# Optimization experiments

Measured on AMD Instinct MI355X. Metric: run time of the kernel, lower is better.

The kernel has to match this reference:

```python
import jax, jax.numpy as jnp
import numpy as np

H = 20          # n_hidden
D_IN = 64       # max_len_input (encoder GRU input size)
VOCAB = 128     # decoder_dict_size
B = 8192
S = 128
MAX_DEC = 6


def _gru_cell(x, h, W_ih, W_hh, b_ih, b_hh):
    # PyTorch GRU cell: gates ordered [r, z, n]
    gi = x @ W_ih.T + b_ih
    gh = h @ W_hh.T + b_hh
    ir, iz, inn = jnp.split(gi, 3, axis=-1)
    hr, hz, hn = jnp.split(gh, 3, axis=-1)
    r = jax.nn.sigmoid(ir + hr)
    z = jax.nn.sigmoid(iz + hz)
    n = jnp.tanh(inn + r * hn)
    return (1.0 - z) * n + z * h


def setup_inputs() -> dict:
    key = jax.random.key(0)
    ks = jax.random.split(key, 32)
    s = 0.1
    p = {}
    p["x"] = jax.random.normal(ks[0], (B, S, D_IN), dtype=jnp.float32)
    # encoder GRU (2 layers)
    p["enc_Wih0"] = jax.random.normal(ks[1], (3 * H, D_IN)) * s
    p["enc_Whh0"] = jax.random.normal(ks[2], (3 * H, H)) * s
    p["enc_bih0"] = jax.random.normal(ks[3], (3 * H,)) * s
    p["enc_bhh0"] = jax.random.normal(ks[4], (3 * H,)) * s
    p["enc_Wih1"] = jax.random.normal(ks[5], (3 * H, H)) * s
    p["enc_Whh1"] = jax.random.normal(ks[6], (3 * H, H)) * s
    p["enc_bih1"] = jax.random.normal(ks[7], (3 * H,)) * s
    p["enc_bhh1"] = jax.random.normal(ks[8], (3 * H,)) * s
    # decoder GRU (2 layers, input size H)
    p["dec_Wih0"] = jax.random.normal(ks[9], (3 * H, H)) * s
    p["dec_Whh0"] = jax.random.normal(ks[10], (3 * H, H)) * s
    p["dec_bih0"] = jax.random.normal(ks[11], (3 * H,)) * s
    p["dec_bhh0"] = jax.random.normal(ks[12], (3 * H,)) * s
    p["dec_Wih1"] = jax.random.normal(ks[13], (3 * H, H)) * s
    p["dec_Whh1"] = jax.random.normal(ks[14], (3 * H, H)) * s
    p["dec_bih1"] = jax.random.normal(ks[15], (3 * H,)) * s
    p["dec_bhh1"] = jax.random.normal(ks[16], (3 * H,)) * s
    # embedding / attention / output heads
    p["emb"] = jax.random.normal(ks[17], (VOCAB, H)) * s
    p["q_W"] = jax.random.normal(ks[18], (H, H)) * s
    p["q_b"] = jax.random.normal(ks[19], (H,)) * s
    p["comb_W"] = jax.random.normal(ks[20], (H, 2 * H)) * s
    p["comb_b"] = jax.random.normal(ks[21], (H,)) * s
    p["out_W"] = jax.random.normal(ks[22], (VOCAB, H)) * s
    p["out_b"] = jax.random.normal(ks[23], (VOCAB,)) * s
    return p


def reference(x, enc_Wih0, enc_Whh0, enc_bih0, enc_bhh0,
              enc_Wih1, enc_Whh1, enc_bih1, enc_bhh1,
              dec_Wih0, dec_Whh0, dec_bih0, dec_bhh0,
              dec_Wih1, dec_Whh1, dec_bih1, dec_bhh1,
              emb, q_W, q_b, comb_W, comb_b, out_W, out_b):
    b = x.shape[0]
    h0 = jnp.zeros((b, H), x.dtype)
    h1 = jnp.zeros((b, H), x.dtype)

    def enc_step(carry, xt):
        c0, c1 = carry
        c0 = _gru_cell(xt, c0, enc_Wih0, enc_Whh0, enc_bih0, enc_bhh0)
        c1 = _gru_cell(c0, c1, enc_Wih1, enc_Whh1, enc_bih1, enc_bhh1)
        return (c0, c1), c1

    (h0, h1), enc_out = jax.lax.scan(enc_step, (h0, h1), jnp.swapaxes(x, 0, 1))
    encoded = jnp.swapaxes(enc_out, 0, 1)  # [B, S, H]

    vec_in = jnp.zeros((b,), dtype=jnp.int32)
    logits_list, attn_list = [], []
    d0, d1 = h0, h1  # hidden carried from encoder
    for _ in range(MAX_DEC):
        e = emb[vec_in]                                 # [B, H]
        d0 = _gru_cell(e, d0, dec_Wih0, dec_Whh0, dec_bih0, dec_bhh0)
        d1 = _gru_cell(d0, d1, dec_Wih1, dec_Whh1, dec_bih1, dec_bhh1)
        buf = d1                                        # decoder output at this step
        query = buf @ q_W.T + q_b                       # [B, H]
        scores = jnp.einsum('bh,bsh->bs', query, encoded)
        w = jax.nn.softmax(scores, axis=1)              # [B, S]
        a = jnp.einsum('bs,bsh->bh', w, encoded)        # attention context
        comb = jnp.concatenate([buf, a], axis=1) @ comb_W.T + comb_b
        logits = comb @ out_W.T + out_b                 # [B, VOCAB]
        logits_list.append(logits)
        attn_list.append(w)
        vec_in = jnp.argmax(logits, axis=1)
    vec_out = jnp.stack(logits_list, axis=1)            # [B, 6, VOCAB]
    hidden = jnp.stack([d0, d1], axis=0)                # [2, B, H]
    attention_weights = jnp.stack(attn_list, axis=0)    # [6, B, S]
    return vec_out, hidden, attention_weights
```

## Files before the change

kernel.cpp:

```cpp
#include <hip/hip_runtime.h>


#define HN 20
#define DIN 64
#define NVOCAB 128
#define NB 8192
#define NS 128
#define NDEC 6

#define HID_OFF (NB * NDEC * NVOCAB)
#define ATTN_OFF (HID_OFF + 2 * NB * HN)

__device__ __forceinline__ float sigf(float x) {
    return 1.0f / (1.0f + __expf(-x));
}

__global__ __launch_bounds__(512, 8)
void enc_kernel(const float* __restrict__ x,
                const float* __restrict__ Wih0, const float* __restrict__ Whh0,
                const float* __restrict__ bih0, const float* __restrict__ bhh0,
                const float* __restrict__ Wih1, const float* __restrict__ Whh1,
                const float* __restrict__ bih1, const float* __restrict__ bhh1,
                float* __restrict__ enc, float* __restrict__ hf0,
                float* __restrict__ hf1)
{
    __shared__ __align__(16) float W0[60][68];
    __shared__ __align__(16) float U0[60][20];
    __shared__ __align__(16) float W1[60][20];
    __shared__ __align__(16) float U1[60][20];
    __shared__ float bi0[60], bh0[60], bi1[60], bh1[60];
    __shared__ __align__(16) float xs[8][68];
    __shared__ __align__(16) float h0s[8][24];
    __shared__ __align__(16) float h1s[8][24];
    __shared__ float gA[80][8];
    __shared__ float gB[80][8];

    const int tid  = threadIdx.x;
    const int bloc = tid & 7;
    const int r    = tid >> 3;
    const int sb   = tid >> 6;
    const int si   = tid & 63;
    const int bid  = (int)blockIdx.x;
    const int gblk = (bid & 7) * 128 + (bid >> 3);
    const int b0   = gblk * 8;

    for (int idx = tid; idx < 60 * 64; idx += 512)
        W0[idx >> 6][idx & 63] = Wih0[idx];
    for (int idx = tid; idx < 60 * 20; idx += 512) {
        (&U0[0][0])[idx] = Whh0[idx];
        (&W1[0][0])[idx] = Wih1[idx];
        (&U1[0][0])[idx] = Whh1[idx];
    }
    if (tid < 60) {
        bi0[tid] = bih0[tid]; bh0[tid] = bhh0[tid];
        bi1[tid] = bih1[tid]; bh1[tid] = bhh1[tid];
    }
    for (int idx = tid; idx < 8 * 24; idx += 512) {
        (&h0s[0][0])[idx] = 0.0f;
        (&h1s[0][0])[idx] = 0.0f;
    }
    xs[sb][si] = x[(b0 + sb) * (NS * DIN) + si];
    __syncthreads();

    for (int i = 0; i <= NS; ++i) {
        float pf = 0.0f;
        const bool havepf = (i <= NS - 2);
        if (havepf)
            pf = x[((b0 + sb) * NS + i + 1) * DIN + si];

        const bool g0 = (i < NS)  && (r < 60);
        const bool g1 = (i >= 1)  && (r < 60);
        if (g0) {
            float ax = bi0[r];
            #pragma unroll
            for (int q = 0; q < 16; ++q) {
                float4 wv = *(const float4*)(&W0[r][4 * q]);
                float4 xv = *(const float4*)(&xs[bloc][4 * q]);
                ax += wv.x * xv.x + wv.y * xv.y + wv.z * xv.z + wv.w * xv.w;
            }
            float ah = bh0[r];
            #pragma unroll
            for (int q = 0; q < 5; ++q) {
                float4 uv = *(const float4*)(&U0[r][4 * q]);
                float4 hv = *(const float4*)(&h0s[bloc][4 * q]);
                ah += uv.x * hv.x + uv.y * hv.y + uv.z * hv.z + uv.w * hv.w;
            }
            if (r < 40) gA[r][bloc] = ax + ah;
            else { gA[r][bloc] = ax; gA[r + 20][bloc] = ah; }
        }
        if (g1) {
            float bx = bi1[r];
            #pragma unroll
            for (int q = 0; q < 5; ++q) {
                float4 wv = *(const float4*)(&W1[r][4 * q]);
                float4 hv = *(const float4*)(&h0s[bloc][4 * q]);
                bx += wv.x * hv.x + wv.y * hv.y + wv.z * hv.z + wv.w * hv.w;
            }
            float bh = bh1[r];
            #pragma unroll
            for (int q = 0; q < 5; ++q) {
                float4 uv = *(const float4*)(&U1[r][4 * q]);
                float4 hv = *(const float4*)(&h1s[bloc][4 * q]);
                bh += uv.x * hv.x + uv.y * hv.y + uv.z * hv.z + uv.w * hv.w;
            }
            if (r < 40) gB[r][bloc] = bx + bh;
            else { gB[r][bloc] = bx; gB[r + 20][bloc] = bh; }
        }
        __syncthreads();

        if (havepf) xs[sb][si] = pf;
        if (r < HN) {
            if (i < NS) {
                float rr = sigf(gA[r][bloc]);
                float z  = sigf(gA[20 + r][bloc]);
                float n  = tanhf(gA[40 + r][bloc] + rr * gA[60 + r][bloc]);
                float hnew = (1.0f - z) * n + z * h0s[bloc][r];
                h0s[bloc][r] = hnew;
                if (i == NS - 1) hf0[(b0 + bloc) * HN + r] = hnew;
            }
            if (i >= 1) {
                int t1 = i - 1;
                float rr = sigf(gB[r][bloc]);
                float z  = sigf(gB[20 + r][bloc]);
                float n  = tanhf(gB[40 + r][bloc] + rr * gB[60 + r][bloc]);
                float hnew = (1.0f - z) * n + z * h1s[bloc][r];
                h1s[bloc][r] = hnew;
                enc[(t1 * HN + r) * NB + b0 + bloc] = hnew;
                if (t1 == NS - 1) hf1[(b0 + bloc) * HN + r] = hnew;
            }
        }
        __syncthreads();
    }
}

__global__ __launch_bounds__(1024, 4)
void dec_kernel(const float* __restrict__ dWih0, const float* __restrict__ dWhh0,
                const float* __restrict__ dbih0, const float* __restrict__ dbhh0,
                const float* __restrict__ dWih1, const float* __restrict__ dWhh1,
                const float* __restrict__ dbih1, const float* __restrict__ dbhh1,
                const float* __restrict__ emb,  const float* __restrict__ qW,
                const float* __restrict__ qb,   const float* __restrict__ combW,
                const float* __restrict__ combb, const float* __restrict__ outW,
                const float* __restrict__ outb,
                const float* __restrict__ enc, const float* __restrict__ hf0,
                const float* __restrict__ hf1, float* __restrict__ out)
{
    __shared__ __align__(16) float el[NS * 164];
    __shared__ float ssb[NS * 9];
    __shared__ __align__(16) float Wih0s[60][20], Whh0s[60][20];
    __shared__ __align__(16) float Wih1s[60][20], Whh1s[60][20];
    __shared__ __align__(16) float qWs[20][20];
    __shared__ __align__(16) float combWs[20][40];
    __shared__ __align__(16) float outWs[128][20];
    __shared__ __align__(16) float embs[128][20];
    __shared__ float bi0s[60], bh0s[60], bi1s[60], bh1s[60];
    __shared__ float qbs[20], cbbs[20], outbs[128];
    __shared__ float hd0[8][24], hd1[8][24];
    __shared__ float gsd[80][8];
    __shared__ float qs[8][24];
    __shared__ float combp[8][24];
    __shared__ float cxp[4][20][8];
    __shared__ float pm[16][8];
    __shared__ int   pix[16][8];
    __shared__ float Ms[8], Sv[8];
    __shared__ int   toks[8];

    const int tid  = threadIdx.x;
    const int bloc = tid & 7;
    const int r    = tid >> 3;
    const int wv   = tid >> 6;
    const int bid  = (int)blockIdx.x;
    const int gblk = (bid & 7) * 128 + (bid >> 3);
    const int b0   = gblk * 8;

    for (int idx = tid; idx < 60 * 20; idx += 1024) {
        (&Wih0s[0][0])[idx] = dWih0[idx];
        (&Whh0s[0][0])[idx] = dWhh0[idx];
        (&Wih1s[0][0])[idx] = dWih1[idx];
        (&Whh1s[0][0])[idx] = dWhh1[idx];
    }
    for (int idx = tid; idx < 400; idx += 1024) (&qWs[0][0])[idx] = qW[idx];
    for (int idx = tid; idx < 800; idx += 1024) (&combWs[0][0])[idx] = combW[idx];
    for (int idx = tid; idx < 2560; idx += 1024) {
        (&outWs[0][0])[idx] = outW[idx];
        (&embs[0][0])[idx]  = emb[idx];
    }
    if (tid < 60) {
        bi0s[tid] = dbih0[tid]; bh0s[tid] = dbhh0[tid];
        bi1s[tid] = dbih1[tid]; bh1s[tid] = dbhh1[tid];
    }
    if (tid < 20) { qbs[tid] = qb[tid]; cbbs[tid] = combb[tid]; }
    if (tid < 128) outbs[tid] = outb[tid];
    for (int idx = tid; idx < 8 * HN; idx += 1024) {
        int bb = idx & 7, k = idx >> 3;
        hd0[bb][k] = hf0[(b0 + bb) * HN + k];
        hd1[bb][k] = hf1[(b0 + bb) * HN + k];
    }
    if (tid < 8) toks[tid] = 0;
    for (int idx = tid; idx < NS * HN * 2; idx += 1024) {
        int tk = idx >> 1, q = idx & 1;
        int t = tk / HN, k = tk % HN;
        float4 v = *(const float4*)(enc + (size_t)tk * NB + b0 + 4 * q);
        *(float4*)(&el[t * 164 + k * 8 + 4 * q]) = v;
    }
    __syncthreads();

    for (int s = 0; s < NDEC; ++s) {
        if (r < 60) {
            const float* er = &embs[toks[bloc]][0];
            float ax = bi0s[r], ah = bh0s[r];
            #pragma unroll
            for (int i = 0; i < HN; ++i) {
                ax += Wih0s[r][i] * er[i];
                ah += Whh0s[r][i] * hd0[bloc][i];
            }
            if (r < 40) gsd[r][bloc] = ax + ah;
            else { gsd[r][bloc] = ax; gsd[r + 20][bloc] = ah; }
        }
        __syncthreads();
        if (r < HN) {
            float rr = sigf(gsd[r][bloc]);
            float z  = sigf(gsd[20 + r][bloc]);
            float n  = tanhf(gsd[40 + r][bloc] + rr * gsd[60 + r][bloc]);
            hd0[bloc][r] = (1.0f - z) * n + z * hd0[bloc][r];
        }
        __syncthreads();
        if (r < 60) {
            float ax = bi1s[r], ah = bh1s[r];
            #pragma unroll
            for (int i = 0; i < HN; ++i) {
                ax += Wih1s[r][i] * hd0[bloc][i];
                ah += Whh1s[r][i] * hd1[bloc][i];
            }
            if (r < 40) gsd[r][bloc] = ax + ah;
            else { gsd[r][bloc] = ax; gsd[r + 20][bloc] = ah; }
        }
        __syncthreads();
        if (r < HN) {
            float rr = sigf(gsd[r][bloc]);
            float z  = sigf(gsd[20 + r][bloc]);
            float n  = tanhf(gsd[40 + r][bloc] + rr * gsd[60 + r][bloc]);
            hd1[bloc][r] = (1.0f - z) * n + z * hd1[bloc][r];
        }
        __syncthreads();
        if (r < HN) {
            float a = qbs[r];
            #pragma unroll
            for (int i = 0; i < HN; ++i) a += qWs[r][i] * hd1[bloc][i];
            qs[bloc][r] = a;
        } else if (r < 2 * HN) {
            int k = r - HN;
            float a = cbbs[k];
            #pragma unroll
            for (int i = 0; i < HN; ++i) a += combWs[k][i] * hd1[bloc][i];
            combp[bloc][k] = a;
        }
        __syncthreads();
        float sc = 0.0f;
        #pragma unroll
        for (int k = 0; k < HN; ++k)
            sc += qs[bloc][k] * el[r * 164 + k * 8 + bloc];
        {
            float m = sc;
            m = fmaxf(m, __shfl_xor(m, 8));
            m = fmaxf(m, __shfl_xor(m, 16));
            m = fmaxf(m, __shfl_xor(m, 32));
            if ((tid & 63) < 8) pm[wv][bloc] = m;
        }
        __syncthreads();
        if (tid < 8) {
            float m = pm[0][tid];
            #pragma unroll
            for (int w2 = 1; w2 < 16; ++w2) m = fmaxf(m, pm[w2][tid]);
            Ms[tid] = m;
        }
        __syncthreads();
        float ev = __expf(sc - Ms[bloc]);
        ssb[r * 9 + bloc] = ev;
        {
            float sm = ev;
            sm += __shfl_xor(sm, 8);
            sm += __shfl_xor(sm, 16);
            sm += __shfl_xor(sm, 32);
            if ((tid & 63) < 8) pm[wv][bloc] = sm;
        }
        __syncthreads();
        if (tid < 8) {
            float sm = pm[0][tid];
            #pragma unroll
            for (int w2 = 1; w2 < 16; ++w2) sm += pm[w2][tid];
            Sv[tid] = 1.0f / sm;
        }
        __syncthreads();
        {
            int vb = tid >> 7, vt = tid & 127;
            out[(size_t)ATTN_OFF + (size_t)s * NB * NS + (size_t)(b0 + vb) * NS + vt]
                = ssb[vt * 9 + vb] * Sv[vb];
        }
        if (r < 80) {
            int ch = r / 20, k = r - 20 * ch;
            int t0 = ch * 32;
            float acc = 0.0f;
            for (int u = 0; u < 32; ++u)
                acc += ssb[(t0 + u) * 9 + bloc] * el[(t0 + u) * 164 + k * 8 + bloc];
            cxp[ch][k][bloc] = acc;
        }
        __syncthreads();
        if (r < HN) {
            float a = combp[bloc][r];
            float inv = Sv[bloc];
            #pragma unroll
            for (int i = 0; i < HN; ++i) {
                float cx = (cxp[0][i][bloc] + cxp[1][i][bloc]
                          + cxp[2][i][bloc] + cxp[3][i][bloc]) * inv;
                a += combWs[r][HN + i] * cx;
            }
            combp[bloc][r] = a;
        }
        __syncthreads();
        {
            float lg = outbs[r];
            #pragma unroll
            for (int k = 0; k < HN; ++k) lg += outWs[r][k] * combp[bloc][k];
            ssb[r * 9 + bloc] = lg;
            float bv = lg; int bi2 = r;
            #pragma unroll
            for (int d = 8; d <= 32; d <<= 1) {
                float ov = __shfl_xor(bv, d);
                int   oi = __shfl_xor(bi2, d);
                if (ov > bv || (ov == bv && oi < bi2)) { bv = ov; bi2 = oi; }
            }
            if ((tid & 63) < 8) { pm[wv][bloc] = bv; pix[wv][bloc] = bi2; }
        }
        __syncthreads();
        {
            int vb = tid >> 7, vt = tid & 127;
            out[(size_t)(b0 + vb) * (NDEC * NVOCAB) + s * NVOCAB + vt]
                = ssb[vt * 9 + vb];
        }
        if (tid < 8) {
            float bv = pm[0][tid]; int bi2 = pix[0][tid];
            #pragma unroll
            for (int w2 = 1; w2 < 16; ++w2) {
                float ov = pm[w2][tid]; int oi = pix[w2][tid];
                if (ov > bv || (ov == bv && oi < bi2)) { bv = ov; bi2 = oi; }
            }
            toks[tid] = bi2;
        }
        __syncthreads();
    }

    for (int idx = tid; idx < 8 * HN; idx += 1024) {
        int bb = idx & 7, k = idx >> 3;
        out[HID_OFF + (b0 + bb) * HN + k] = hd0[bb][k];
        out[HID_OFF + NB * HN + (b0 + bb) * HN + k] = hd1[bb][k];
    }
}

extern "C" void kernel_launch(void* const* d_in, const int* in_sizes, int n_in,
                              void* d_out, int out_size, void* d_ws, size_t ws_size,
                              hipStream_t stream)
{
    const float* x        = (const float*)d_in[0];
    const float* eWih0    = (const float*)d_in[1];
    const float* eWhh0    = (const float*)d_in[2];
    const float* ebih0    = (const float*)d_in[3];
    const float* ebhh0    = (const float*)d_in[4];
    const float* eWih1    = (const float*)d_in[5];
    const float* eWhh1    = (const float*)d_in[6];
    const float* ebih1    = (const float*)d_in[7];
    const float* ebhh1    = (const float*)d_in[8];
    const float* dWih0    = (const float*)d_in[9];
    const float* dWhh0    = (const float*)d_in[10];
    const float* dbih0    = (const float*)d_in[11];
    const float* dbhh0    = (const float*)d_in[12];
    const float* dWih1    = (const float*)d_in[13];
    const float* dWhh1    = (const float*)d_in[14];
    const float* dbih1    = (const float*)d_in[15];
    const float* dbhh1    = (const float*)d_in[16];
    const float* emb      = (const float*)d_in[17];
    const float* qW       = (const float*)d_in[18];
    const float* qb       = (const float*)d_in[19];
    const float* combW    = (const float*)d_in[20];
    const float* combb    = (const float*)d_in[21];
    const float* outW     = (const float*)d_in[22];
    const float* outb     = (const float*)d_in[23];

    const size_t need = ((size_t)NS * HN * NB + 2 * (size_t)NB * HN) * sizeof(float);
    if (ws_size < need) return;

    float* ws  = (float*)d_ws;
    float* enc = ws;
    float* hf0 = ws + (size_t)NS * HN * NB;
    float* hf1 = hf0 + (size_t)NB * HN;

    enc_kernel<<<1024, 512, 0, stream>>>(x, eWih0, eWhh0, ebih0, ebhh0,
                                         eWih1, eWhh1, ebih1, ebhh1,
                                         enc, hf0, hf1);
    dec_kernel<<<1024, 1024, 0, stream>>>(dWih0, dWhh0, dbih0, dbhh0,
                                          dWih1, dWhh1, dbih1, dbhh1,
                                          emb, qW, qb, combW, combb, outW, outb,
                                          enc, hf0, hf1, (float*)d_out);
}
```

Baseline: 1.092 ms.

## Rewrite decoder as one-wavefront-per-batch with register-resident encoder outputs

The decoder changes from 1024-thread blocks covering 8 batch rows to 256-thread blocks where each 64-lane wavefront owns one batch row. That row's encoder outputs sit in registers, and softmax, context reduction and argmax run on wavefront shuffles, which removes most shared-memory staging and block-wide barriers. The encoder output layout becomes batch-major so each wavefront reads contiguous memory, and the final hidden of layer 1 is read from the last encoder step instead of a separate buffer. The encoder gets FMA chains with two accumulators and biases held in registers. The cost is much higher register pressure (around 40+ live floats for encodings plus 20 for cx) and decoder weights read from global/L1 instead of shared memory.

```diff
diff --git a/kernel.cpp b/kernel.cpp
--- a/kernel.cpp
+++ b/kernel.cpp
@@ -21,14 +21,12 @@
                 const float* __restrict__ bih0, const float* __restrict__ bhh0,
                 const float* __restrict__ Wih1, const float* __restrict__ Whh1,
                 const float* __restrict__ bih1, const float* __restrict__ bhh1,
-                float* __restrict__ enc, float* __restrict__ hf0,
-                float* __restrict__ hf1)
+                float* __restrict__ enc, float* __restrict__ hf0)
 {
     __shared__ __align__(16) float W0[60][68];
     __shared__ __align__(16) float U0[60][20];
     __shared__ __align__(16) float W1[60][20];
     __shared__ __align__(16) float U1[60][20];
-    __shared__ float bi0[60], bh0[60], bi1[60], bh1[60];
     __shared__ __align__(16) float xs[8][68];
     __shared__ __align__(16) float h0s[8][24];
     __shared__ __align__(16) float h1s[8][24];
@@ -51,9 +49,10 @@
         (&W1[0][0])[idx] = Wih1[idx];
         (&U1[0][0])[idx] = Whh1[idx];
     }
-    if (tid < 60) {
-        bi0[tid] = bih0[tid]; bh0[tid] = bhh0[tid];
-        bi1[tid] = bih1[tid]; bh1[tid] = bhh1[tid];
+    float bi0r = 0.f, bh0r = 0.f, bi1r = 0.f, bh1r = 0.f;
+    if (r < 60) {
+        bi0r = bih0[r]; bh0r = bhh0[r];
+        bi1r = bih1[r]; bh1r = bhh1[r];
     }
     for (int idx = tid; idx < 8 * 24; idx += 512) {
         (&h0s[0][0])[idx] = 0.0f;
@@ -68,40 +67,49 @@
         if (havepf)
             pf = x[((b0 + sb) * NS + i + 1) * DIN + si];
 
-        const bool g0 = (i < NS)  && (r < 60);
-        const bool g1 = (i >= 1)  && (r < 60);
+        const bool g0 = (i < NS) && (r < 60);
+        const bool g1 = (i >= 1) && (r < 60);
         if (g0) {
-            float ax = bi0[r];
-            #pragma unroll
-            for (int q = 0; q < 16; ++q) {
+            float ax0 = bi0r, ax1 = 0.0f;
+            #pragma unroll
+            for (int q = 0; q < 16; q += 2) {
                 float4 wv = *(const float4*)(&W0[r][4 * q]);
                 float4 xv = *(const float4*)(&xs[bloc][4 * q]);
-                ax += wv.x * xv.x + wv.y * xv.y + wv.z * xv.z + wv.w * xv.w;
-            }
-            float ah = bh0[r];
+                ax0 = fmaf(wv.x, xv.x, ax0); ax0 = fmaf(wv.y, xv.y, ax0);
+                ax0 = fmaf(wv.z, xv.z, ax0); ax0 = fmaf(wv.w, xv.w, ax0);
+                float4 wu = *(const float4*)(&W0[r][4 * q + 4]);
+                float4 xu = *(const float4*)(&xs[bloc][4 * q + 4]);
+                ax1 = fmaf(wu.x, xu.x, ax1); ax1 = fmaf(wu.y, xu.y, ax1);
+                ax1 = fmaf(wu.z, xu.z, ax1); ax1 = fmaf(wu.w, xu.w, ax1);
+            }
+            float ax = ax0 + ax1;
+            float ah = bh0r;
             #pragma unroll
             for (int q = 0; q < 5; ++q) {
                 float4 uv = *(const float4*)(&U0[r][4 * q]);
                 float4 hv = *(const float4*)(&h0s[bloc][4 * q]);
-                ah += uv.x * hv.x + uv.y * hv.y + uv.z * hv.z + uv.w * hv.w;
+                ah = fmaf(uv.x, hv.x, ah); ah = fmaf(uv.y, hv.y, ah);
+                ah = fmaf(uv.z, hv.z, ah); ah = fmaf(uv.w, hv.w, ah);
             }
             if (r < 40) gA[r][bloc] = ax + ah;
             else { gA[r][bloc] = ax; gA[r + 20][bloc] = ah; }
         }
         if (g1) {
-            float bx = bi1[r];
+            float bx = bi1r;
             #pragma unroll
             for (int q = 0; q < 5; ++q) {
                 float4 wv = *(const float4*)(&W1[r][4 * q]);
                 float4 hv = *(const float4*)(&h0s[bloc][4 * q]);
-                bx += wv.x * hv.x + wv.y * hv.y + wv.z * hv.z + wv.w * hv.w;
-            }
-            float bh = bh1[r];
+                bx = fmaf(wv.x, hv.x, bx); bx = fmaf(wv.y, hv.y, bx);
+                bx = fmaf(wv.z, hv.z, bx); bx = fmaf(wv.w, hv.w, bx);
+            }
+            float bh = bh1r;
             #pragma unroll
             for (int q = 0; q < 5; ++q) {
                 float4 uv = *(const float4*)(&U1[r][4 * q]);
                 float4 hv = *(const float4*)(&h1s[bloc][4 * q]);
-                bh += uv.x * hv.x + uv.y * hv.y + uv.z * hv.z + uv.w * hv.w;
+                bh = fmaf(uv.x, hv.x, bh); bh = fmaf(uv.y, hv.y, bh);
+                bh = fmaf(uv.z, hv.z, bh); bh = fmaf(uv.w, hv.w, bh);
             }
             if (r < 40) gB[r][bloc] = bx + bh;
             else { gB[r][bloc] = bx; gB[r + 20][bloc] = bh; }
@@ -125,15 +133,14 @@
                 float n  = tanhf(gB[40 + r][bloc] + rr * gB[60 + r][bloc]);
                 float hnew = (1.0f - z) * n + z * h1s[bloc][r];
                 h1s[bloc][r] = hnew;
-                enc[(t1 * HN + r) * NB + b0 + bloc] = hnew;
-                if (t1 == NS - 1) hf1[(b0 + bloc) * HN + r] = hnew;
+                enc[(size_t)(b0 + bloc) * (NS * HN) + t1 * HN + r] = hnew;
             }
         }
         __syncthreads();
     }
 }
 
-__global__ __launch_bounds__(1024, 4)
+__global__ __launch_bounds__(256)
 void dec_kernel(const float* __restrict__ dWih0, const float* __restrict__ dWhh0,
                 const float* __restrict__ dbih0, const float* __restrict__ dbhh0,
                 const float* __restrict__ dWih1, const float* __restrict__ dWhh1,
@@ -143,217 +150,207 @@
                 const float* __restrict__ combb, const float* __restrict__ outW,
                 const float* __restrict__ outb,
                 const float* __restrict__ enc, const float* __restrict__ hf0,
-                const float* __restrict__ hf1, float* __restrict__ out)
+                float* __restrict__ out)
 {
-    __shared__ __align__(16) float el[NS * 164];
-    __shared__ float ssb[NS * 9];
-    __shared__ __align__(16) float Wih0s[60][20], Whh0s[60][20];
-    __shared__ __align__(16) float Wih1s[60][20], Whh1s[60][20];
-    __shared__ __align__(16) float qWs[20][20];
-    __shared__ __align__(16) float combWs[20][40];
-    __shared__ __align__(16) float outWs[128][20];
-    __shared__ __align__(16) float embs[128][20];
-    __shared__ float bi0s[60], bh0s[60], bi1s[60], bh1s[60];
-    __shared__ float qbs[20], cbbs[20], outbs[128];
-    __shared__ float hd0[8][24], hd1[8][24];
-    __shared__ float gsd[80][8];
-    __shared__ float qs[8][24];
-    __shared__ float combp[8][24];
-    __shared__ float cxp[4][20][8];
-    __shared__ float pm[16][8];
-    __shared__ int   pix[16][8];
-    __shared__ float Ms[8], Sv[8];
-    __shared__ int   toks[8];
+    __shared__ __align__(16) float hb0[4][20];
+    __shared__ __align__(16) float hb1[4][20];
+    __shared__ __align__(16) float qsh[4][20];
+    __shared__ __align__(16) float csh[4][20];
 
     const int tid  = threadIdx.x;
-    const int bloc = tid & 7;
-    const int r    = tid >> 3;
+    const int l    = tid & 63;
     const int wv   = tid >> 6;
     const int bid  = (int)blockIdx.x;
-    const int gblk = (bid & 7) * 128 + (bid >> 3);
-    const int b0   = gblk * 8;
-
-    for (int idx = tid; idx < 60 * 20; idx += 1024) {
-        (&Wih0s[0][0])[idx] = dWih0[idx];
-        (&Whh0s[0][0])[idx] = dWhh0[idx];
-        (&Wih1s[0][0])[idx] = dWih1[idx];
-        (&Whh1s[0][0])[idx] = dWhh1[idx];
-    }
-    for (int idx = tid; idx < 400; idx += 1024) (&qWs[0][0])[idx] = qW[idx];
-    for (int idx = tid; idx < 800; idx += 1024) (&combWs[0][0])[idx] = combW[idx];
-    for (int idx = tid; idx < 2560; idx += 1024) {
-        (&outWs[0][0])[idx] = outW[idx];
-        (&embs[0][0])[idx]  = emb[idx];
-    }
-    if (tid < 60) {
-        bi0s[tid] = dbih0[tid]; bh0s[tid] = dbhh0[tid];
-        bi1s[tid] = dbih1[tid]; bh1s[tid] = dbhh1[tid];
-    }
-    if (tid < 20) { qbs[tid] = qb[tid]; cbbs[tid] = combb[tid]; }
-    if (tid < 128) outbs[tid] = outb[tid];
-    for (int idx = tid; idx < 8 * HN; idx += 1024) {
-        int bb = idx & 7, k = idx >> 3;
-        hd0[bb][k] = hf0[(b0 + bb) * HN + k];
-        hd1[bb][k] = hf1[(b0 + bb) * HN + k];
-    }
-    if (tid < 8) toks[tid] = 0;
-    for (int idx = tid; idx < NS * HN * 2; idx += 1024) {
-        int tk = idx >> 1, q = idx & 1;
-        int t = tk / HN, k = tk % HN;
-        float4 v = *(const float4*)(enc + (size_t)tk * NB + b0 + 4 * q);
-        *(float4*)(&el[t * 164 + k * 8 + 4 * q]) = v;
-    }
+    const int gblk = (bid & 7) * 256 + (bid >> 3);
+    const int b    = gblk * 4 + wv;
+
+    float e0[20], e1[20];
+    const float* src = enc + (size_t)b * (NS * HN);
+    #pragma unroll
+    for (int q = 0; q < 5; ++q) {
+        float4 v = *(const float4*)(src + l * HN + 4 * q);
+        e0[4*q+0] = v.x; e0[4*q+1] = v.y; e0[4*q+2] = v.z; e0[4*q+3] = v.w;
+        float4 u = *(const float4*)(src + (64 + l) * HN + 4 * q);
+        e1[4*q+0] = u.x; e1[4*q+1] = u.y; e1[4*q+2] = u.z; e1[4*q+3] = u.w;
+    }
+    float h0v = 0.0f, h1v = 0.0f;
+    if (l < HN) {
+        h0v = hf0[b * HN + l];
+        h1v = src[127 * HN + l];
+        hb0[wv][l] = h0v;
+        hb1[wv][l] = h1v;
+    }
+    int tok = 0;
     __syncthreads();
 
     for (int s = 0; s < NDEC; ++s) {
-        if (r < 60) {
-            const float* er = &embs[toks[bloc]][0];
-            float ax = bi0s[r], ah = bh0s[r];
-            #pragma unroll
-            for (int i = 0; i < HN; ++i) {
-                ax += Wih0s[r][i] * er[i];
-                ah += Whh0s[r][i] * hd0[bloc][i];
-            }
-            if (r < 40) gsd[r][bloc] = ax + ah;
-            else { gsd[r][bloc] = ax; gsd[r + 20][bloc] = ah; }
-        }
-        __syncthreads();
-        if (r < HN) {
-            float rr = sigf(gsd[r][bloc]);
-            float z  = sigf(gsd[20 + r][bloc]);
-            float n  = tanhf(gsd[40 + r][bloc] + rr * gsd[60 + r][bloc]);
-            hd0[bloc][r] = (1.0f - z) * n + z * hd0[bloc][r];
-        }
-        __syncthreads();
-        if (r < 60) {
-            float ax = bi1s[r], ah = bh1s[r];
-            #pragma unroll
-            for (int i = 0; i < HN; ++i) {
-                ax += Wih1s[r][i] * hd0[bloc][i];
-                ah += Whh1s[r][i] * hd1[bloc][i];
-            }
-            if (r < 40) gsd[r][bloc] = ax + ah;
-            else { gsd[r][bloc] = ax; gsd[r + 20][bloc] = ah; }
-        }
-        __syncthreads();
-        if (r < HN) {
-            float rr = sigf(gsd[r][bloc]);
-            float z  = sigf(gsd[20 + r][bloc]);
-            float n  = tanhf(gsd[40 + r][bloc] + rr * gsd[60 + r][bloc]);
-            hd1[bloc][r] = (1.0f - z) * n + z * hd1[bloc][r];
-        }
-        __syncthreads();
-        if (r < HN) {
-            float a = qbs[r];
-            #pragma unroll
-            for (int i = 0; i < HN; ++i) a += qWs[r][i] * hd1[bloc][i];
-            qs[bloc][r] = a;
-        } else if (r < 2 * HN) {
-            int k = r - HN;
-            float a = cbbs[k];
-            #pragma unroll
-            for (int i = 0; i < HN; ++i) a += combWs[k][i] * hd1[bloc][i];
-            combp[bloc][k] = a;
-        }
-        __syncthreads();
-        float sc = 0.0f;
-        #pragma unroll
-        for (int k = 0; k < HN; ++k)
-            sc += qs[bloc][k] * el[r * 164 + k * 8 + bloc];
+        const float* ep = emb + tok * HN;
+
+        float g = 0.0f, axn = 0.0f, ahn = 0.0f;
+        if (l < 60) {
+            const float* wi = dWih0 + l * HN;
+            const float* wh = dWhh0 + l * HN;
+            float ax = dbih0[l], ah = dbhh0[l];
+            #pragma unroll
+            for (int q = 0; q < 5; ++q) {
+                float4 w4 = *(const float4*)(wi + 4 * q);
+                ax = fmaf(w4.x, ep[4*q+0], ax); ax = fmaf(w4.y, ep[4*q+1], ax);
+                ax = fmaf(w4.z, ep[4*q+2], ax); ax = fmaf(w4.w, ep[4*q+3], ax);
+                float4 u4 = *(const float4*)(wh + 4 * q);
+                float4 h4 = *(const float4*)(&hb0[wv][4 * q]);
+                ah = fmaf(u4.x, h4.x, ah); ah = fmaf(u4.y, h4.y, ah);
+                ah = fmaf(u4.z, h4.z, ah); ah = fmaf(u4.w, h4.w, ah);
+            }
+            g = ax + ah; axn = ax; ahn = ah;
+        }
+        float zg  = __shfl(g,   l + 20);
+        float inn = __shfl(axn, l + 40);
+        float hnn = __shfl(ahn, l + 40);
+        if (l < HN) {
+            float rr = sigf(g);
+            float zz = sigf(zg);
+            float nn = tanhf(inn + rr * hnn);
+            h0v = (1.0f - zz) * nn + zz * h0v;
+            hb0[wv][l] = h0v;
+        }
+        __syncthreads();
+
+        g = 0.0f; axn = 0.0f; ahn = 0.0f;
+        if (l < 60) {
+            const float* wi = dWih1 + l * HN;
+            const float* wh = dWhh1 + l * HN;
+            float ax = dbih1[l], ah = dbhh1[l];
+            #pragma unroll
+            for (int q = 0; q < 5; ++q) {
+                float4 w4 = *(const float4*)(wi + 4 * q);
+                float4 h4 = *(const float4*)(&hb0[wv][4 * q]);
+                ax = fmaf(w4.x, h4.x, ax); ax = fmaf(w4.y, h4.y, ax);
+                ax = fmaf(w4.z, h4.z, ax); ax = fmaf(w4.w, h4.w, ax);
+                float4 u4 = *(const float4*)(wh + 4 * q);
+                float4 g4 = *(const float4*)(&hb1[wv][4 * q]);
+                ah = fmaf(u4.x, g4.x, ah); ah = fmaf(u4.y, g4.y, ah);
+                ah = fmaf(u4.z, g4.z, ah); ah = fmaf(u4.w, g4.w, ah);
+            }
+            g = ax + ah; axn = ax; ahn = ah;
+        }
+        zg  = __shfl(g,   l + 20);
+        inn = __shfl(axn, l + 40);
+        hnn = __shfl(ahn, l + 40);
+        if (l < HN) {
+            float rr = sigf(g);
+            float zz = sigf(zg);
+            float nn = tanhf(inn + rr * hnn);
+            h1v = (1.0f - zz) * nn + zz * h1v;
+            hb1[wv][l] = h1v;
+        }
+        __syncthreads();
+
+        float cbv = 0.0f;
+        if (l < HN) {
+            float qv = qb[l];
+            const float* qr = qW + l * HN;
+            #pragma unroll
+            for (int q = 0; q < 5; ++q) {
+                float4 w4 = *(const float4*)(qr + 4 * q);
+                float4 h4 = *(const float4*)(&hb1[wv][4 * q]);
+                qv = fmaf(w4.x, h4.x, qv); qv = fmaf(w4.y, h4.y, qv);
+                qv = fmaf(w4.z, h4.z, qv); qv = fmaf(w4.w, h4.w, qv);
+            }
+            qsh[wv][l] = qv;
+        } else if (l < 2 * HN) {
+            int k2 = l - HN;
+            cbv = combb[k2];
+            const float* cr = combW + k2 * 2 * HN;
+            #pragma unroll
+            for (int q = 0; q < 5; ++q) {
+                float4 w4 = *(const float4*)(cr + 4 * q);
+                float4 h4 = *(const float4*)(&hb1[wv][4 * q]);
+                cbv = fmaf(w4.x, h4.x, cbv); cbv = fmaf(w4.y, h4.y, cbv);
+                cbv = fmaf(w4.z, h4.z, cbv); cbv = fmaf(w4.w, h4.w, cbv);
+            }
+        }
+        __syncthreads();
+
+        float s0 = 0.0f, s1 = 0.0f;
+        #pragma unroll
+        for (int k = 0; k < HN; ++k) {
+            float qk = qsh[wv][k];
+            s0 = fmaf(qk, e0[k], s0);
+            s1 = fmaf(qk, e1[k], s1);
+        }
+        float m = fmaxf(s0, s1);
+        #pragma unroll
+        for (int d = 1; d < 64; d <<= 1) m = fmaxf(m, __shfl_xor(m, d));
+        float x0 = __expf(s0 - m), x1 = __expf(s1 - m);
+        float sm = x0 + x1;
+        #pragma unroll
+        for (int d = 1; d < 64; d <<= 1) sm += __shfl_xor(sm, d);
+        float inv = 1.0f / sm;
+        float w0 = x0 * inv, w1 = x1 * inv;
         {
-            float m = sc;
-            m = fmaxf(m, __shfl_xor(m, 8));
-            m = fmaxf(m, __shfl_xor(m, 16));
-            m = fmaxf(m, __shfl_xor(m, 32));
-            if ((tid & 63) < 8) pm[wv][bloc] = m;
-        }
-        __syncthreads();
-        if (tid < 8) {
-            float m = pm[0][tid];
-            #pragma unroll
-            for (int w2 = 1; w2 < 16; ++w2) m = fmaxf(m, pm[w2][tid]);
-            Ms[tid] = m;
-        }
-        __syncthreads();
-        float ev = __expf(sc - Ms[bloc]);
-        ssb[r * 9 + bloc] = ev;
+            size_t abase = (size_t)ATTN_OFF + (size_t)s * NB * NS + (size_t)b * NS;
+            out[abase + l]      = w0;
+            out[abase + 64 + l] = w1;
+        }
+
+        float cx[20];
+        #pragma unroll
+        for (int k = 0; k < HN; ++k) cx[k] = fmaf(w1, e1[k], w0 * e0[k]);
+        #pragma unroll
+        for (int d = 1; d < 64; d <<= 1) {
+            #pragma unroll
+            for (int k = 0; k < HN; ++k) cx[k] += __shfl_xor(cx[k], d);
+        }
+
+        float cpre = __shfl(cbv, l + 20);
+        if (l < HN) {
+            float cv = cpre;
+            const float* cr = combW + l * 2 * HN + HN;
+            #pragma unroll
+            for (int q = 0; q < 5; ++q) {
+                float4 w4 = *(const float4*)(cr + 4 * q);
+                cv = fmaf(w4.x, cx[4*q+0], cv); cv = fmaf(w4.y, cx[4*q+1], cv);
+                cv = fmaf(w4.z, cx[4*q+2], cv); cv = fmaf(w4.w, cx[4*q+3], cv);
+            }
+            csh[wv][l] = cv;
+        }
+        __syncthreads();
+
+        float lg0 = outb[l], lg1 = outb[64 + l];
         {
-            float sm = ev;
-            sm += __shfl_xor(sm, 8);
-            sm += __shfl_xor(sm, 16);
-            sm += __shfl_xor(sm, 32);
-            if ((tid & 63) < 8) pm[wv][bloc] = sm;
-        }
-        __syncthreads();
-        if (tid < 8) {
-            float sm = pm[0][tid];
-            #pragma unroll
-            for (int w2 = 1; w2 < 16; ++w2) sm += pm[w2][tid];
-            Sv[tid] = 1.0f / sm;
-        }
-        __syncthreads();
+            const float* o0 = outW + l * HN;
+            const float* o1 = outW + (64 + l) * HN;
+            #pragma unroll
+            for (int q = 0; q < 5; ++q) {
+                float4 a4 = *(const float4*)(o0 + 4 * q);
+                float4 b4 = *(const float4*)(o1 + 4 * q);
+                float4 c4 = *(const float4*)(&csh[wv][4 * q]);
+                lg0 = fmaf(a4.x, c4.x, lg0); lg0 = fmaf(a4.y, c4.y, lg0);
+                lg0 = fmaf(a4.z, c4.z, lg0); lg0 = fmaf(a4.w, c4.w, lg0);
+                lg1 = fmaf(b4.x, c4.x, lg1); lg1 = fmaf(b4.y, c4.y, lg1);
+                lg1 = fmaf(b4.z, c4.z, lg1); lg1 = fmaf(b4.w, c4.w, lg1);
+            }
+        }
         {
-            int vb = tid >> 7, vt = tid & 127;
-            out[(size_t)ATTN_OFF + (size_t)s * NB * NS + (size_t)(b0 + vb) * NS + vt]
-                = ssb[vt * 9 + vb] * Sv[vb];
-        }
-        if (r < 80) {
-            int ch = r / 20, k = r - 20 * ch;
-            int t0 = ch * 32;
-            float acc = 0.0f;
-            for (int u = 0; u < 32; ++u)
-                acc += ssb[(t0 + u) * 9 + bloc] * el[(t0 + u) * 164 + k * 8 + bloc];
-            cxp[ch][k][bloc] = acc;
-        }
-        __syncthreads();
-        if (r < HN) {
-            float a = combp[bloc][r];
-            float inv = Sv[bloc];
-            #pragma unroll
-            for (int i = 0; i < HN; ++i) {
-                float cx = (cxp[0][i][bloc] + cxp[1][i][bloc]
-                          + cxp[2][i][bloc] + cxp[3][i][bloc]) * inv;
-                a += combWs[r][HN + i] * cx;
-            }
-            combp[bloc][r] = a;
-        }
-        __syncthreads();
-        {
-            float lg = outbs[r];
-            #pragma unroll
-            for (int k = 0; k < HN; ++k) lg += outWs[r][k] * combp[bloc][k];
-            ssb[r * 9 + bloc] = lg;
-            float bv = lg; int bi2 = r;
-            #pragma unroll
-            for (int d = 8; d <= 32; d <<= 1) {
-                float ov = __shfl_xor(bv, d);
-                int   oi = __shfl_xor(bi2, d);
-                if (ov > bv || (ov == bv && oi < bi2)) { bv = ov; bi2 = oi; }
-            }
-            if ((tid & 63) < 8) { pm[wv][bloc] = bv; pix[wv][bloc] = bi2; }
-        }
-        __syncthreads();
-        {
-            int vb = tid >> 7, vt = tid & 127;
-            out[(size_t)(b0 + vb) * (NDEC * NVOCAB) + s * NVOCAB + vt]
-                = ssb[vt * 9 + vb];
-        }
-        if (tid < 8) {
-            float bv = pm[0][tid]; int bi2 = pix[0][tid];
-            #pragma unroll
-            for (int w2 = 1; w2 < 16; ++w2) {
-                float ov = pm[w2][tid]; int oi = pix[w2][tid];
-                if (ov > bv || (ov == bv && oi < bi2)) { bv = ov; bi2 = oi; }
-            }
-            toks[tid] = bi2;
-        }
-        __syncthreads();
-    }
-
-    for (int idx = tid; idx < 8 * HN; idx += 1024) {
-        int bb = idx & 7, k = idx >> 3;
-        out[HID_OFF + (b0 + bb) * HN + k] = hd0[bb][k];
-        out[HID_OFF + NB * HN + (b0 + bb) * HN + k] = hd1[bb][k];
+            size_t lbase = (size_t)b * (NDEC * NVOCAB) + (size_t)s * NVOCAB;
+            out[lbase + l]      = lg0;
+            out[lbase + 64 + l] = lg1;
+        }
+        float bv = lg0; int bi2 = l;
+        if (lg1 > bv) { bv = lg1; bi2 = 64 + l; }
+        #pragma unroll
+        for (int d = 1; d < 64; d <<= 1) {
+            float ov = __shfl_xor(bv, d);
+            int   oi = __shfl_xor(bi2, d);
+            if (ov > bv || (ov == bv && oi < bi2)) { bv = ov; bi2 = oi; }
+        }
+        tok = __builtin_amdgcn_readfirstlane(bi2);
+        __syncthreads();
+    }
+
+    if (l < HN) {
+        out[HID_OFF + (size_t)b * HN + l]           = h0v;
+        out[HID_OFF + NB * HN + (size_t)b * HN + l] = h1v;
     }
 }
 
@@ -386,19 +383,18 @@
     const float* outW     = (const float*)d_in[22];
     const float* outb     = (const float*)d_in[23];
 
-    const size_t need = ((size_t)NS * HN * NB + 2 * (size_t)NB * HN) * sizeof(float);
+    const size_t need = ((size_t)NB * NS * HN + (size_t)NB * HN) * sizeof(float);
     if (ws_size < need) return;
 
     float* ws  = (float*)d_ws;
     float* enc = ws;
-    float* hf0 = ws + (size_t)NS * HN * NB;
-    float* hf1 = hf0 + (size_t)NB * HN;
+    float* hf0 = ws + (size_t)NB * NS * HN;
 
     enc_kernel<<<1024, 512, 0, stream>>>(x, eWih0, eWhh0, ebih0, ebhh0,
                                          eWih1, eWhh1, ebih1, ebhh1,
-                                         enc, hf0, hf1);
-    dec_kernel<<<1024, 1024, 0, stream>>>(dWih0, dWhh0, dbih0, dbhh0,
-                                          dWih1, dWhh1, dbih1, dbhh1,
-                                          emb, qW, qb, combW, combb, outW, outb,
-                                          enc, hf0, hf1, (float*)d_out);
+                                         enc, hf0);
+    dec_kernel<<<2048, 256, 0, stream>>>(dWih0, dWhh0, dbih0, dbhh0,
+                                         dWih1, dWhh1, dbih1, dbhh1,
+                                         emb, qW, qb, combW, combb, outW, outb,
+                                         enc, hf0, (float*)d_out);
 }
```

Measured after the change: 1.003 ms. 1.09x faster.
